# Optimization experiments

Measured on AMD Instinct MI355X. Metric: run time of the kernel, lower is better.

Reference implementation:

```python
import jax, jax.numpy as jnp
import numpy as np

N_DIM = 2  # number of trailing feature columns treated as coordinates


def setup_inputs() -> dict:
    key = jax.random.key(0)
    k1, k2, k3, k4 = jax.random.split(key, 4)
    B, N, F, O = 32, 1024, 64, 128
    x = jax.random.normal(k1, (B, N, F), dtype=jnp.float32)
    mask = (jax.random.uniform(k2, (B, N)) < 0.8).astype(jnp.float32)
    # A has shape ((F+1)*2 - 1, O) = (2F+1, O) per build()
    A = jax.random.normal(k3, ((F + 1) * 2 - 1, O), dtype=jnp.float32) * 0.05
    b = jax.random.normal(k4, (O,), dtype=jnp.float32) * 0.05
    return {"x": x, "mask": mask, "A": A, "b": b}


def reference(x, mask, A, b):
    # x: [B,N,F], mask: [B,N], A: [2F+1,O], b: [O]
    # TF tiles: a[b,i,j] = x[b,j]; b_t[b,i,j] = x[b,i]
    coords = x[:, :, -N_DIM:]                              # [B,N,d]
    # diff[b,i,j] = coords[b,j] - coords[b,i]  (ca - cb in TF)
    diff = coords[:, None, :, :] - coords[:, :, None, :]   # [B,N,N,d]
    dist = jnp.sum(diff * diff, axis=-1)                   # [B,N,N] (i,j)
    w = jnp.exp(-10.0 * dist)                              # [B,N,N]
    # TF: s[b,i,j,:] = concat(x[b,j], dist[b,i,j]) * w[b,i,j] * mask[b,j]
    #     ss[b,j]    = sum_i s[b,i,j]
    wsum = jnp.sum(w, axis=1)                              # [B,N] indexed by j
    dwsum = jnp.sum(dist * w, axis=1)                      # [B,N] indexed by j
    m = mask[..., None]                                    # [B,N,1]
    ss_feat = x * wsum[..., None] * m                      # [B,N,F]
    ss_dist = dwsum[..., None] * m                         # [B,N,1]
    ss = jnp.concatenate([ss_feat, ss_dist], axis=-1)      # [B,N,F+1]
    # subtract self term: xx = concat(x, 0)
    xx = jnp.concatenate([x, jnp.zeros_like(x[..., :1])], axis=-1)
    ss = ss - xx
    h = jnp.concatenate([x, ss], axis=-1)                  # [B,N,2F+1]
    out = (h @ A + b) * m                                  # [B,N,O]
    return out
```

## Files before the change

### kernel.cpp

```cpp
#include <hip/hip_runtime.h>
#include <hip/hip_bf16.h>

typedef __attribute__((ext_vector_type(8))) short bf16x8;
typedef __attribute__((ext_vector_type(4))) float f32x4;
typedef __attribute__((ext_vector_type(16))) float f32x16;

#define NN 1024
#define FF 64
#define OO 128

#define LOG2E    1.4426950408889634f
#define C20L     (20.0f * LOG2E)
#define C10L     (10.0f * LOG2E)
#define NEG_LN2_10 (-0.06931471805599453f)
#define BF1      ((short)0x3F80)

__device__ __forceinline__ short bfh(float f) {
    __hip_bfloat16 h = __float2bfloat16(f);
    return *reinterpret_cast<short*>(&h);
}
__device__ __forceinline__ float bf2f(short s) {
    union { unsigned u; float f; } v; v.u = ((unsigned)(unsigned short)s) << 16;
    return v.f;
}

__global__ __launch_bounds__(512) void gnn_fused_kernel(
    const float* __restrict__ x, const float* __restrict__ mask,
    const float* __restrict__ A, const float* __restrict__ bias,
    float* __restrict__ out)
{
    __shared__ __align__(16) short  ivec[NN * 8];
    __shared__ __align__(16) bf16x8 jlo[128], jhi[128];
    __shared__ __align__(16) bf16x8 cst;
    __shared__ __align__(16) float part_w[2][2][64];
    __shared__ __align__(16) float part_t[2][2][64];

    const int tid = threadIdx.x;
    const int w   = tid >> 6;
    const int l   = tid & 63;
    const int l16 = l & 15;
    const int lh  = l >> 4;

    const int bid = blockIdx.x;
    const int b     = (bid & 7) * 4 + (bid >> 6);
    const int jbase = ((bid >> 3) & 7) * 128;
    const int rowbase_g = b * NN + jbase;
    const float* xb = x + (size_t)b * NN * FF;

    #pragma unroll
    for (int q = 0; q < 2; ++q) {
        int p = tid + q * 512;
        float2 c2 = *(const float2*)(xb + (size_t)p * FF + (FF - 2));
        float vx = C20L * c2.x, vy = C20L * c2.y;
        float r2 = fmaf(c2.x, c2.x, c2.y * c2.y);
        float u  = -C10L * r2;
        short vxh = bfh(vx); short vxl = bfh(vx - bf2f(vxh));
        short vyh = bfh(vy); short vyl = bfh(vy - bf2f(vyh));
        short uh  = bfh(u);  short ul  = bfh(u  - bf2f(uh));
        bf16x8 iv = {vxh, vxl, vxh, vyh, vyl, vyh, uh, ul};
        *(bf16x8*)&ivec[p * 8] = iv;
        unsigned jloc = (unsigned)(p - jbase);
        if (jloc < 128u) {
            short xh = bfh(c2.x); short xl = bfh(c2.x - bf2f(xh));
            short yh = bfh(c2.y); short yl = bfh(c2.y - bf2f(yh));
            jlo[jloc] = (bf16x8){xh, xh, xl, yh, yh, yl, BF1, BF1};
            jhi[jloc] = (bf16x8){uh, ul, 0, 0, 0, 0, 0, 0};
        }
    }
    if (tid == 0) cst = (bf16x8){BF1, BF1, 0, 0, 0, 0, 0, 0};

    __syncthreads();

    if (w >= 4) {
        const int jh_ = (w - 4) & 1;
        const int ih  = (w - 4) >> 1;
        const int j31 = l & 31;
        const f32x16 Z = {0.f,0.f,0.f,0.f,0.f,0.f,0.f,0.f,
                          0.f,0.f,0.f,0.f,0.f,0.f,0.f,0.f};
        for (int t = 0; t < 2; ++t) {
            const int jj = t * 64 + 32 * jh_ + j31;
            const bf16x8* bp = (l < 32) ? &jlo[jj] : &jhi[jj];
            bf16x8 Bj = *bp;
            float aw0 = 0.f, aw1 = 0.f, at0 = 0.f, at1 = 0.f;
            __builtin_amdgcn_s_setprio(1);
            #pragma unroll
            for (int c = 0; c < 16; ++c) {
                const bf16x8* ap = (l < 32)
                    ? (const bf16x8*)&ivec[(ih * 512 + c * 32 + j31) * 8]
                    : &cst;
                bf16x8 Af = *ap;
                f32x16 S = __builtin_amdgcn_mfma_f32_32x32x16_bf16(Af, Bj, Z, 0, 0, 0);
                #pragma unroll
                for (int r = 0; r < 16; r += 2) {
                    float p2a = S[r], p2b = S[r + 1];
                    float wa = __builtin_amdgcn_exp2f(p2a);
                    float wb = __builtin_amdgcn_exp2f(p2b);
                    aw0 += wa;                 aw1 += wb;
                    at0 = fmaf(p2a, wa, at0);  at1 = fmaf(p2b, wb, at1);
                }
            }
            __builtin_amdgcn_s_setprio(0);
            float aw = aw0 + aw1, at = at0 + at1;
            aw += __shfl_xor(aw, 32);
            at += __shfl_xor(at, 32);
            if (l < 32) {
                part_w[t][ih][32 * jh_ + j31] = aw;
                part_t[t][ih][32 * jh_ + j31] = at;
            }
            __syncthreads();
        }
    } else {
        const int colbase = (w & 3) * 32;
        const f32x4 Z4 = {0.f, 0.f, 0.f, 0.f};
        f32x4 acc[4][2][2];

        bf16x8 Bh[2][2][2];
        #pragma unroll
        for (int cg = 0; cg < 2; ++cg)
            #pragma unroll
            for (int g = 0; g < 2; ++g)
                #pragma unroll
                for (int q = 0; q < 2; ++q) {
                    const float* ap = A + (size_t)(g * FF + 32 * q + 8 * lh) * OO
                                      + colbase + 16 * cg + l16;
                    #pragma unroll
                    for (int e = 0; e < 8; ++e)
                        Bh[cg][g][q][e] = bfh(ap[(size_t)e * OO]);
                }
        float a2v[2], bbv[2];
        #pragma unroll
        for (int cg = 0; cg < 2; ++cg) {
            a2v[cg] = A[(size_t)(2 * FF) * OO + colbase + 16 * cg + l16];
            bbv[cg] = bias[colbase + 16 * cg + l16];
        }

        for (int t = 0; t < 2; ++t) {
            const float* xpb = x + (size_t)(rowbase_g + t * 64 + l16) * FF + 8 * lh;
            #pragma unroll
            for (int ms = 0; ms < 4; ++ms) {
                const float* _p = xpb + ms * 16 * FF;
                float4 v0 = *(const float4*)(_p);
                float4 v1 = *(const float4*)(_p + 4);
                float4 v2 = *(const float4*)(_p + 32);
                float4 v3 = *(const float4*)(_p + 36);
                float src[16] = {v0.x, v0.y, v0.z, v0.w, v1.x, v1.y, v1.z, v1.w,
                                 v2.x, v2.y, v2.z, v2.w, v3.x, v3.y, v3.z, v3.w};
                bf16x8 Xh[2];
                #pragma unroll
                for (int q = 0; q < 2; ++q)
                    #pragma unroll
                    for (int e = 0; e < 8; ++e)
                        Xh[q][e] = bfh(src[q * 8 + e]);
                #pragma unroll
                for (int cg = 0; cg < 2; ++cg)
                    #pragma unroll
                    for (int g = 0; g < 2; ++g) {
                        acc[ms][cg][g] = __builtin_amdgcn_mfma_f32_16x16x32_bf16(
                            Xh[0], Bh[cg][g][0], Z4, 0, 0, 0);
                        acc[ms][cg][g] = __builtin_amdgcn_mfma_f32_16x16x32_bf16(
                            Xh[1], Bh[cg][g][1], acc[ms][cg][g], 0, 0, 0);
                    }
            }

            __syncthreads();

            #pragma unroll
            for (int ms = 0; ms < 4; ++ms) {
                const int rl  = 16 * ms + 4 * lh;
                const int erg = rowbase_g + t * 64 + rl;
                float4 mk = *(const float4*)(mask + erg);
                float4 w0 = *(const float4*)&part_w[t][0][rl];
                float4 w1 = *(const float4*)&part_w[t][1][rl];
                float4 t0 = *(const float4*)&part_t[t][0][rl];
                float4 t1 = *(const float4*)&part_t[t][1][rl];
                float mks[4] = {mk.x, mk.y, mk.z, mk.w};
                float wvs[4] = {w0.x + w1.x, w0.y + w1.y, w0.z + w1.z, w0.w + w1.w};
                float dvs[4] = {(t0.x + t1.x) * NEG_LN2_10, (t0.y + t1.y) * NEG_LN2_10,
                                (t0.z + t1.z) * NEG_LN2_10, (t0.w + t1.w) * NEG_LN2_10};
                #pragma unroll
                for (int r = 0; r < 4; ++r) {
                    const int row = erg + r;
                    const float m   = mks[r];
                    const float s   = wvs[r] * m - 1.f;
                    const float dwm = dvs[r] * m;
                    #pragma unroll
                    for (int cg = 0; cg < 2; ++cg) {
                        float val = acc[ms][cg][0][r] + s * acc[ms][cg][1][r]
                                  + dwm * a2v[cg] + bbv[cg];
                        out[(size_t)row * OO + colbase + 16 * cg + l16] = val * m;
                    }
                }
            }
        }
    }
}

extern "C" void kernel_launch(void* const* d_in, const int* in_sizes, int n_in,
                              void* d_out, int out_size, void* d_ws, size_t ws_size,
                              hipStream_t stream)
{
    const float* x    = (const float*)d_in[0];
    const float* mask = (const float*)d_in[1];
    const float* A    = (const float*)d_in[2];
    const float* bias = (const float*)d_in[3];
    float* out = (float*)d_out;

    gnn_fused_kernel<<<dim3(256), dim3(512), 0, stream>>>(x, mask, A, bias, out);
}
```

Measured before the change: 15.67 us.

## Double block size to 1024 threads, splitting pairwise and GEMM work across more waves

Raises the workgroup from 512 to 1024 threads. Eight waves now compute the pairwise exp sums, each covering a quarter of the i range instead of half, and eight waves do the output GEMM at 16 columns each instead of 32. The partial-sum arrays grow to four slices and are combined in the epilogue. The aim is more in-flight waves per block to shorten the critical path of the exp-heavy loop, at the cost of more barrier participants and lower per-wave register budgets.

```diff
diff --git a/kernel.cpp b/kernel.cpp
--- a/kernel.cpp
+++ b/kernel.cpp
@@ -24,7 +24,7 @@
     return v.f;
 }
 
-__global__ __launch_bounds__(512) void gnn_fused_kernel(
+__global__ __launch_bounds__(1024, 4) void gnn_fused_kernel(
     const float* __restrict__ x, const float* __restrict__ mask,
     const float* __restrict__ A, const float* __restrict__ bias,
     float* __restrict__ out)
@@ -32,8 +32,8 @@
     __shared__ __align__(16) short  ivec[NN * 8];
     __shared__ __align__(16) bf16x8 jlo[128], jhi[128];
     __shared__ __align__(16) bf16x8 cst;
-    __shared__ __align__(16) float part_w[2][2][64];
-    __shared__ __align__(16) float part_t[2][2][64];
+    __shared__ __align__(16) float part_w[2][4][64];
+    __shared__ __align__(16) float part_t[2][4][64];
 
     const int tid = threadIdx.x;
     const int w   = tid >> 6;
@@ -47,9 +47,8 @@
     const int rowbase_g = b * NN + jbase;
     const float* xb = x + (size_t)b * NN * FF;
 
-    #pragma unroll
-    for (int q = 0; q < 2; ++q) {
-        int p = tid + q * 512;
+    {
+        int p = tid;
         float2 c2 = *(const float2*)(xb + (size_t)p * FF + (FF - 2));
         float vx = C20L * c2.x, vy = C20L * c2.y;
         float r2 = fmaf(c2.x, c2.x, c2.y * c2.y);
@@ -66,14 +65,15 @@
             jlo[jloc] = (bf16x8){xh, xh, xl, yh, yh, yl, BF1, BF1};
             jhi[jloc] = (bf16x8){uh, ul, 0, 0, 0, 0, 0, 0};
         }
+        if (tid == 0) cst = (bf16x8){BF1, BF1, 0, 0, 0, 0, 0, 0};
     }
-    if (tid == 0) cst = (bf16x8){BF1, BF1, 0, 0, 0, 0, 0, 0};
 
     __syncthreads();
 
-    if (w >= 4) {
-        const int jh_ = (w - 4) & 1;
-        const int ih  = (w - 4) >> 1;
+    if (w >= 8) {
+        const int idx = w - 8;
+        const int jh_ = idx & 1;
+        const int iq  = idx >> 1;
         const int j31 = l & 31;
         const f32x16 Z = {0.f,0.f,0.f,0.f,0.f,0.f,0.f,0.f,
                           0.f,0.f,0.f,0.f,0.f,0.f,0.f,0.f};
@@ -84,9 +84,9 @@
             float aw0 = 0.f, aw1 = 0.f, at0 = 0.f, at1 = 0.f;
             __builtin_amdgcn_s_setprio(1);
             #pragma unroll
-            for (int c = 0; c < 16; ++c) {
+            for (int c = 0; c < 8; ++c) {
                 const bf16x8* ap = (l < 32)
-                    ? (const bf16x8*)&ivec[(ih * 512 + c * 32 + j31) * 8]
+                    ? (const bf16x8*)&ivec[(iq * 256 + c * 32 + j31) * 8]
                     : &cst;
                 bf16x8 Af = *ap;
                 f32x16 S = __builtin_amdgcn_mfma_f32_32x32x16_bf16(Af, Bj, Z, 0, 0, 0);
@@ -104,35 +104,29 @@
             aw += __shfl_xor(aw, 32);
             at += __shfl_xor(at, 32);
             if (l < 32) {
-                part_w[t][ih][32 * jh_ + j31] = aw;
-                part_t[t][ih][32 * jh_ + j31] = at;
+                part_w[t][iq][32 * jh_ + j31] = aw;
+                part_t[t][iq][32 * jh_ + j31] = at;
             }
             __syncthreads();
         }
     } else {
-        const int colbase = (w & 3) * 32;
+        const int colbase = w * 16;
         const f32x4 Z4 = {0.f, 0.f, 0.f, 0.f};
-        f32x4 acc[4][2][2];
-
-        bf16x8 Bh[2][2][2];
+        f32x4 acc[4][2];
+
+        bf16x8 Bh[2][2];
         #pragma unroll
-        for (int cg = 0; cg < 2; ++cg)
-            #pragma unroll
-            for (int g = 0; g < 2; ++g)
-                #pragma unroll
-                for (int q = 0; q < 2; ++q) {
-                    const float* ap = A + (size_t)(g * FF + 32 * q + 8 * lh) * OO
-                                      + colbase + 16 * cg + l16;
-                    #pragma unroll
-                    for (int e = 0; e < 8; ++e)
-                        Bh[cg][g][q][e] = bfh(ap[(size_t)e * OO]);
-                }
-        float a2v[2], bbv[2];
-        #pragma unroll
-        for (int cg = 0; cg < 2; ++cg) {
-            a2v[cg] = A[(size_t)(2 * FF) * OO + colbase + 16 * cg + l16];
-            bbv[cg] = bias[colbase + 16 * cg + l16];
-        }
+        for (int g = 0; g < 2; ++g)
+            #pragma unroll
+            for (int q = 0; q < 2; ++q) {
+                const float* ap = A + (size_t)(g * FF + 32 * q + 8 * lh) * OO
+                                  + colbase + l16;
+                #pragma unroll
+                for (int e = 0; e < 8; ++e)
+                    Bh[g][q][e] = bfh(ap[(size_t)e * OO]);
+            }
+        const float a2v = A[(size_t)(2 * FF) * OO + colbase + l16];
+        const float bbv = bias[colbase + l16];
 
         for (int t = 0; t < 2; ++t) {
             const float* xpb = x + (size_t)(rowbase_g + t * 64 + l16) * FF + 8 * lh;
@@ -152,14 +146,12 @@
                     for (int e = 0; e < 8; ++e)
                         Xh[q][e] = bfh(src[q * 8 + e]);
                 #pragma unroll
-                for (int cg = 0; cg < 2; ++cg)
-                    #pragma unroll
-                    for (int g = 0; g < 2; ++g) {
-                        acc[ms][cg][g] = __builtin_amdgcn_mfma_f32_16x16x32_bf16(
-                            Xh[0], Bh[cg][g][0], Z4, 0, 0, 0);
-                        acc[ms][cg][g] = __builtin_amdgcn_mfma_f32_16x16x32_bf16(
-                            Xh[1], Bh[cg][g][1], acc[ms][cg][g], 0, 0, 0);
-                    }
+                for (int g = 0; g < 2; ++g) {
+                    acc[ms][g] = __builtin_amdgcn_mfma_f32_16x16x32_bf16(
+                        Xh[0], Bh[g][0], Z4, 0, 0, 0);
+                    acc[ms][g] = __builtin_amdgcn_mfma_f32_16x16x32_bf16(
+                        Xh[1], Bh[g][1], acc[ms][g], 0, 0, 0);
+                }
             }
 
             __syncthreads();
@@ -171,24 +163,30 @@
                 float4 mk = *(const float4*)(mask + erg);
                 float4 w0 = *(const float4*)&part_w[t][0][rl];
                 float4 w1 = *(const float4*)&part_w[t][1][rl];
+                float4 w2 = *(const float4*)&part_w[t][2][rl];
+                float4 w3 = *(const float4*)&part_w[t][3][rl];
                 float4 t0 = *(const float4*)&part_t[t][0][rl];
                 float4 t1 = *(const float4*)&part_t[t][1][rl];
+                float4 t2 = *(const float4*)&part_t[t][2][rl];
+                float4 t3 = *(const float4*)&part_t[t][3][rl];
                 float mks[4] = {mk.x, mk.y, mk.z, mk.w};
-                float wvs[4] = {w0.x + w1.x, w0.y + w1.y, w0.z + w1.z, w0.w + w1.w};
-                float dvs[4] = {(t0.x + t1.x) * NEG_LN2_10, (t0.y + t1.y) * NEG_LN2_10,
-                                (t0.z + t1.z) * NEG_LN2_10, (t0.w + t1.w) * NEG_LN2_10};
+                float wvs[4] = {(w0.x + w1.x) + (w2.x + w3.x),
+                                (w0.y + w1.y) + (w2.y + w3.y),
+                                (w0.z + w1.z) + (w2.z + w3.z),
+                                (w0.w + w1.w) + (w2.w + w3.w)};
+                float dvs[4] = {((t0.x + t1.x) + (t2.x + t3.x)) * NEG_LN2_10,
+                                ((t0.y + t1.y) + (t2.y + t3.y)) * NEG_LN2_10,
+                                ((t0.z + t1.z) + (t2.z + t3.z)) * NEG_LN2_10,
+                                ((t0.w + t1.w) + (t2.w + t3.w)) * NEG_LN2_10};
                 #pragma unroll
                 for (int r = 0; r < 4; ++r) {
                     const int row = erg + r;
                     const float m   = mks[r];
                     const float s   = wvs[r] * m - 1.f;
                     const float dwm = dvs[r] * m;
-                    #pragma unroll
-                    for (int cg = 0; cg < 2; ++cg) {
-                        float val = acc[ms][cg][0][r] + s * acc[ms][cg][1][r]
-                                  + dwm * a2v[cg] + bbv[cg];
-                        out[(size_t)row * OO + colbase + 16 * cg + l16] = val * m;
-                    }
+                    float val = acc[ms][0][r] + s * acc[ms][1][r]
+                              + dwm * a2v + bbv;
+                    out[(size_t)row * OO + colbase + l16] = val * m;
                 }
             }
         }
@@ -205,5 +203,5 @@
     const float* bias = (const float*)d_in[3];
     float* out = (float*)d_out;
 
-    gnn_fused_kernel<<<dim3(256), dim3(512), 0, stream>>>(x, mask, A, bias, out);
-}
+    gnn_fused_kernel<<<dim3(256), dim3(1024), 0, stream>>>(x, mask, A, bias, out);
+}
```

After: 19.59 us. 25.0% more time.

## Prefetch second x tile before barrier and vectorize output stores as float2

Applied to the files above, without the earlier changes.

The GEMM waves now load and convert the second 64-row x tile into registers before waiting on the first barrier, so that global-load latency overlaps the wait for the pairwise-exp waves. The column mapping is also changed so each lane owns two adjacent output columns, letting the epilogue write float2 stores instead of scalar stores. This raises register pressure (an extra 8 bf16x8 values held live) and changes the A-column access pattern to a stride-2 per lane.

```diff
diff --git a/kernel.cpp b/kernel.cpp
--- a/kernel.cpp
+++ b/kernel.cpp
@@ -111,6 +111,7 @@
         }
     } else {
         const int colbase = (w & 3) * 32;
+        const int c2i = colbase + 2 * l16;
         const f32x4 Z4 = {0.f, 0.f, 0.f, 0.f};
         f32x4 acc[4][2][2];
 
@@ -122,7 +123,7 @@
                 #pragma unroll
                 for (int q = 0; q < 2; ++q) {
                     const float* ap = A + (size_t)(g * FF + 32 * q + 8 * lh) * OO
-                                      + colbase + 16 * cg + l16;
+                                      + c2i + cg;
                     #pragma unroll
                     for (int e = 0; e < 8; ++e)
                         Bh[cg][g][q][e] = bfh(ap[(size_t)e * OO]);
@@ -130,12 +131,12 @@
         float a2v[2], bbv[2];
         #pragma unroll
         for (int cg = 0; cg < 2; ++cg) {
-            a2v[cg] = A[(size_t)(2 * FF) * OO + colbase + 16 * cg + l16];
-            bbv[cg] = bias[colbase + 16 * cg + l16];
-        }
-
-        for (int t = 0; t < 2; ++t) {
-            const float* xpb = x + (size_t)(rowbase_g + t * 64 + l16) * FF + 8 * lh;
+            a2v[cg] = A[(size_t)(2 * FF) * OO + c2i + cg];
+            bbv[cg] = bias[c2i + cg];
+        }
+
+        {
+            const float* xpb = x + (size_t)(rowbase_g + l16) * FF + 8 * lh;
             #pragma unroll
             for (int ms = 0; ms < 4; ++ms) {
                 const float* _p = xpb + ms * 16 * FF;
@@ -161,35 +162,97 @@
                             Xh[1], Bh[cg][g][1], acc[ms][cg][g], 0, 0, 0);
                     }
             }
-
-            __syncthreads();
-
+        }
+
+        bf16x8 Xn[4][2];
+        {
+            const float* xpb = x + (size_t)(rowbase_g + 64 + l16) * FF + 8 * lh;
             #pragma unroll
             for (int ms = 0; ms < 4; ++ms) {
-                const int rl  = 16 * ms + 4 * lh;
-                const int erg = rowbase_g + t * 64 + rl;
-                float4 mk = *(const float4*)(mask + erg);
-                float4 w0 = *(const float4*)&part_w[t][0][rl];
-                float4 w1 = *(const float4*)&part_w[t][1][rl];
-                float4 t0 = *(const float4*)&part_t[t][0][rl];
-                float4 t1 = *(const float4*)&part_t[t][1][rl];
-                float mks[4] = {mk.x, mk.y, mk.z, mk.w};
-                float wvs[4] = {w0.x + w1.x, w0.y + w1.y, w0.z + w1.z, w0.w + w1.w};
-                float dvs[4] = {(t0.x + t1.x) * NEG_LN2_10, (t0.y + t1.y) * NEG_LN2_10,
-                                (t0.z + t1.z) * NEG_LN2_10, (t0.w + t1.w) * NEG_LN2_10};
-                #pragma unroll
-                for (int r = 0; r < 4; ++r) {
-                    const int row = erg + r;
-                    const float m   = mks[r];
-                    const float s   = wvs[r] * m - 1.f;
-                    const float dwm = dvs[r] * m;
-                    #pragma unroll
-                    for (int cg = 0; cg < 2; ++cg) {
-                        float val = acc[ms][cg][0][r] + s * acc[ms][cg][1][r]
-                                  + dwm * a2v[cg] + bbv[cg];
-                        out[(size_t)row * OO + colbase + 16 * cg + l16] = val * m;
-                    }
+                const float* _p = xpb + ms * 16 * FF;
+                float4 v0 = *(const float4*)(_p);
+                float4 v1 = *(const float4*)(_p + 4);
+                float4 v2 = *(const float4*)(_p + 32);
+                float4 v3 = *(const float4*)(_p + 36);
+                float src[16] = {v0.x, v0.y, v0.z, v0.w, v1.x, v1.y, v1.z, v1.w,
+                                 v2.x, v2.y, v2.z, v2.w, v3.x, v3.y, v3.z, v3.w};
+                #pragma unroll
+                for (int q = 0; q < 2; ++q)
+                    #pragma unroll
+                    for (int e = 0; e < 8; ++e)
+                        Xn[ms][q][e] = bfh(src[q * 8 + e]);
+            }
+        }
+
+        __syncthreads();
+
+        #pragma unroll
+        for (int ms = 0; ms < 4; ++ms) {
+            const int rl  = 16 * ms + 4 * lh;
+            const int erg = rowbase_g + rl;
+            float4 mk = *(const float4*)(mask + erg);
+            float4 w0 = *(const float4*)&part_w[0][0][rl];
+            float4 w1 = *(const float4*)&part_w[0][1][rl];
+            float4 t0 = *(const float4*)&part_t[0][0][rl];
+            float4 t1 = *(const float4*)&part_t[0][1][rl];
+            float mks[4] = {mk.x, mk.y, mk.z, mk.w};
+            float wvs[4] = {w0.x + w1.x, w0.y + w1.y, w0.z + w1.z, w0.w + w1.w};
+            float dvs[4] = {(t0.x + t1.x) * NEG_LN2_10, (t0.y + t1.y) * NEG_LN2_10,
+                            (t0.z + t1.z) * NEG_LN2_10, (t0.w + t1.w) * NEG_LN2_10};
+            #pragma unroll
+            for (int r = 0; r < 4; ++r) {
+                const int row = erg + r;
+                const float m   = mks[r];
+                const float s   = wvs[r] * m - 1.f;
+                const float dwm = dvs[r] * m;
+                float2 st;
+                st.x = (acc[ms][0][0][r] + s * acc[ms][0][1][r]
+                        + dwm * a2v[0] + bbv[0]) * m;
+                st.y = (acc[ms][1][0][r] + s * acc[ms][1][1][r]
+                        + dwm * a2v[1] + bbv[1]) * m;
+                *(float2*)(out + (size_t)row * OO + c2i) = st;
+            }
+        }
+
+        #pragma unroll
+        for (int ms = 0; ms < 4; ++ms)
+            #pragma unroll
+            for (int cg = 0; cg < 2; ++cg)
+                #pragma unroll
+                for (int g = 0; g < 2; ++g) {
+                    acc[ms][cg][g] = __builtin_amdgcn_mfma_f32_16x16x32_bf16(
+                        Xn[ms][0], Bh[cg][g][0], Z4, 0, 0, 0);
+                    acc[ms][cg][g] = __builtin_amdgcn_mfma_f32_16x16x32_bf16(
+                        Xn[ms][1], Bh[cg][g][1], acc[ms][cg][g], 0, 0, 0);
                 }
+
+        __syncthreads();
+
+        #pragma unroll
+        for (int ms = 0; ms < 4; ++ms) {
+            const int rl  = 16 * ms + 4 * lh;
+            const int erg = rowbase_g + 64 + rl;
+            float4 mk = *(const float4*)(mask + erg);
+            float4 w0 = *(const float4*)&part_w[1][0][rl];
+            float4 w1 = *(const float4*)&part_w[1][1][rl];
+            float4 t0 = *(const float4*)&part_t[1][0][rl];
+            float4 t1 = *(const float4*)&part_t[1][1][rl];
+            float mks[4] = {mk.x, mk.y, mk.z, mk.w};
+            float wvs[4] = {w0.x + w1.x, w0.y + w1.y, w0.z + w1.z, w0.w + w1.w};
+            float dvs[4] = {(t0.x + t1.x) * NEG_LN2_10, (t0.y + t1.y) * NEG_LN2_10,
+                            (t0.z + t1.z) * NEG_LN2_10, (t0.w + t1.w) * NEG_LN2_10};
+            #pragma unroll
+            for (int r = 0; r < 4; ++r) {
+                const int row = erg + r;
+                const float m   = mks[r];
+                const float s   = wvs[r] * m - 1.f;
+                const float dwm = dvs[r] * m;
+                float2 st;
+                st.x = (acc[ms][0][0][r] + s * acc[ms][0][1][r]
+                        + dwm * a2v[0] + bbv[0]) * m;
+                st.y = (acc[ms][1][0][r] + s * acc[ms][1][1][r]
+                        + dwm * a2v[1] + bbv[1]) * m;
+                *(float2*)(out + (size_t)row * OO + c2i) = st;
             }
         }
     }
```

Result: slower. 16.87 us (+7.6%).
